# Performance work log

Hardware: AMD Instinct MI355X
Metric: run time of the kernel (lower is better)

The kernel has to match this reference:

```python
import jax, jax.numpy as jnp
import numpy as np

N_U = 50000
N_I = 50000
E = 800000
E_LBL = 200000
D_IN = 128
HID = 256
OUT = 128


def setup_inputs() -> dict:
    key = jax.random.key(0)
    ks = jax.random.split(key, 32)
    def glorot(k, shp):
        fan = shp[0] + shp[1]
        return jax.random.uniform(k, shp, jnp.float32, -1.0, 1.0) * np.sqrt(6.0 / fan)
    inp = {
        'x_user': jax.random.normal(ks[0], (N_U, D_IN), jnp.float32),
        'x_item': jax.random.normal(ks[1], (N_I, D_IN), jnp.float32),
        'edge_ui': jax.random.randint(ks[2], (2, E), 0, N_U, jnp.int32),
        'edge_iu': jax.random.randint(ks[3], (2, E), 0, N_I, jnp.int32),
        'edge_lbl': jax.random.randint(ks[4], (2, E_LBL), 0, N_U, jnp.int32),
        # layer 0 SAGE params (src_dim=D_IN, dst_dim=D_IN)
        'w_msg_ui0': glorot(ks[5], (D_IN, HID)), 'b_ui0': jnp.zeros((HID,), jnp.float32), 'w_root_ui0': glorot(ks[6], (D_IN, HID)),
        'w_msg_iu0': glorot(ks[7], (D_IN, HID)), 'b_iu0': jnp.zeros((HID,), jnp.float32), 'w_root_iu0': glorot(ks[8], (D_IN, HID)),
        # layer 1 SAGE params (src_dim=HID, dst_dim=HID)
        'w_msg_ui1': glorot(ks[9], (HID, HID)), 'b_ui1': jnp.zeros((HID,), jnp.float32), 'w_root_ui1': glorot(ks[10], (HID, HID)),
        'w_msg_iu1': glorot(ks[11], (HID, HID)), 'b_iu1': jnp.zeros((HID,), jnp.float32), 'w_root_iu1': glorot(ks[12], (HID, HID)),
        # per-node-type output linears on JK concat (2*HID -> OUT)
        'w_lin_u': glorot(ks[13], (2 * HID, OUT)), 'b_lin_u': jnp.zeros((OUT,), jnp.float32),
        'w_lin_i': glorot(ks[14], (2 * HID, OUT)), 'b_lin_i': jnp.zeros((OUT,), jnp.float32),
    }
    return inp


def _sage(x_src, x_dst, edge, w_msg, b_msg, w_root):
    # PyG SAGEConv(aggr='mean'): lin_l(mean_{j in N(i)} x_src[j]) + lin_r(x_dst[i])
    src, dst = edge[0], edge[1]
    n_dst = x_dst.shape[0]
    agg = jax.ops.segment_sum(x_src[src], dst, num_segments=n_dst)          # [n_dst, d_src]
    cnt = jax.ops.segment_sum(jnp.ones((edge.shape[1],), x_src.dtype), dst, num_segments=n_dst)
    mean = agg / jnp.maximum(cnt, 1.0)[:, None]
    return mean @ w_msg + b_msg + x_dst @ w_root


def reference(x_user, x_item, edge_ui, edge_iu, edge_lbl,
              w_msg_ui0, b_ui0, w_root_ui0, w_msg_iu0, b_iu0, w_root_iu0,
              w_msg_ui1, b_ui1, w_root_ui1, w_msg_iu1, b_iu1, w_root_iu1,
              w_lin_u, b_lin_u, w_lin_i, b_lin_i):
    # ----- encode: 2 HeteroConv(SAGEConv) layers -----
    item0 = _sage(x_user, x_item, edge_ui, w_msg_ui0, b_ui0, w_root_ui0)    # user->item
    user0 = _sage(x_item, x_user, edge_iu, b_msg=b_iu0, w_msg=w_msg_iu0, x_src=None, x_dst=None, edge=None, w_root=None) if False else _sage(x_item, x_user, edge_iu, w_msg_iu0, b_iu0, w_root_iu0)  # item->user
    item1 = _sage(user0, item0, edge_ui, w_msg_ui1, b_ui1, w_root_ui1)
    user1 = _sage(item0, user0, edge_iu, w_msg_iu1, b_iu1, w_root_iu1)
    # ----- JumpingKnowledge 'cat' + per-node-type linear -----
    z_user = jnp.concatenate([user0, user1], axis=-1) @ w_lin_u + b_lin_u   # [N_U, OUT]
    z_item = jnp.concatenate([item0, item1], axis=-1) @ w_lin_i + b_lin_i   # [N_I, OUT]
    # ----- decode: dot product over candidate edges (user, buys, item) -----
    pred = jnp.sum(z_user[edge_lbl[0]] * z_item[edge_lbl[1]], axis=-1)      # [E_LBL]
    return pred
```

## Files before the change

### kernel.cpp

```cpp
#include <hip/hip_runtime.h>

#define NU 50000
#define NI 50000
#define NE 800000
#define NLBL 200000
#define DIN 128
#define HID 256
#define DOUT 128

#define NSLICE 128
#define SLICE_SZ 6250
#define QN 12500
#define NQ 4

typedef unsigned short ushort_t;
typedef __attribute__((ext_vector_type(8))) short bf16x8;
typedef __attribute__((ext_vector_type(4))) float f32x4;

__device__ __forceinline__ float bf2f(unsigned int u_shifted) {
    union { unsigned int i; float f; } v;
    v.i = u_shifted;
    return v.f;
}
__device__ __forceinline__ float bf_lo(unsigned int u) { return bf2f(u << 16); }
__device__ __forceinline__ float bf_hi(unsigned int u) { return bf2f(u & 0xffff0000u); }
__device__ __forceinline__ ushort_t f2bf(float f) {
    union { float f; unsigned int i; } v;
    v.f = f;
    unsigned int r = (v.i + 0x7FFFu + ((v.i >> 16) & 1u)) >> 16;
    return (ushort_t)r;
}
__device__ __forceinline__ void load_lds16(const ushort_t* g, ushort_t* s) {
    __builtin_amdgcn_global_load_lds(
        (const __attribute__((address_space(1))) void*)g,
        (__attribute__((address_space(3))) void*)s, 16, 0, 0);
}

#define CVT_PER 782
#define CVT_B (2 * CVT_PER)
#define SA_B 512
#define HIST_B (2 * NSLICE * NQ)

struct P1Args {
    const int *eui, *eiu;
    ushort_t* cnt_s;
    const float *wm_ui1, *wr_ui1, *wm_iu1, *wr_iu1, *lin_i, *lin_u;
    float *G_i, *S_i, *G_u, *S_u;
    int* scan_part;
};

__global__ __launch_bounds__(256) void phase1(P1Args a) {
    __shared__ unsigned int cnt[QN / 2];
    int b = blockIdx.x, t = threadIdx.x;
    if (b < HIST_B) {
        int g = b >> 9, s = (b >> 2) & 127, q = b & 3;
        for (int i = t; i < QN / 2; i += 256) cnt[i] = 0;
        __syncthreads();
        const int* dst = (g ? a.eiu : a.eui) + NE;
        int hbase = q * QN;
        int e0 = s * SLICE_SZ;
        for (int i = e0 + t; i < e0 + SLICE_SZ; i += 256) {
            int d = dst[i] - hbase;
            if ((unsigned)d < (unsigned)QN)
                atomicAdd(&cnt[d >> 1], 1u << ((d & 1) * 16));
        }
        __syncthreads();
        unsigned int* outp = (unsigned int*)(a.cnt_s + ((size_t)(g * NSLICE + s)) * 50000 + hbase);
        for (int i = t; i < QN / 2; i += 256) outp[i] = cnt[i];
    } else if (b < HIST_B + SA_B) {
        int r2 = b - HIST_B;
        int which = r2 >> 7;
        int e = (r2 & 127) * 256 + t;
        int k = e >> 7, n = e & 127;
        const float* W = (which == 0) ? a.wm_ui1 : (which == 1) ? a.wr_ui1
                       : (which == 2) ? a.wm_iu1 : a.wr_iu1;
        const float* L = (which < 2) ? a.lin_i : a.lin_u;
        float* O = (which == 0) ? a.G_i : (which == 1) ? a.S_i
                 : (which == 2) ? a.G_u : a.S_u;
        float s = (which & 1) ? L[k * 128 + n] : 0.f;
#pragma unroll 4
        for (int j = 0; j < HID; ++j) s += W[k * HID + j] * L[(HID + j) * 128 + n];
        O[k * 128 + n] = s;
    } else {
        if (t < 64) a.scan_part[t] = 0;
    }
}

struct K2Args {
    ushort_t* cnt_s;
    int* totals;
    int* scan_part;
    const float *wm_ui0, *wr_ui0, *wm_iu0, *wr_iu0;
    const float *G_i, *S_i, *G_u, *S_u;
    const float *b_ui0, *b_iu0, *b_ui1, *b_iu1, *lin_i, *lin_u, *bl_i, *bl_u;
    ushort_t *VT1_i, *VT2_i, *VT3_i, *VT1_u, *VT2_u, *VT3_u;
    float *bz_i, *bz_u;
    const float* xu; ushort_t* xbu; const float* xi; ushort_t* xbi;
};

__global__ __launch_bounds__(256) void k2_scan_prep_cvt(K2Args a) {
    __shared__ int wsum[4];
    int b = blockIdx.x, t = threadIdx.x;
    if (b < 392) {
        if (b == 0 && t == 0) a.totals[100000] = 2 * NE;
        int idx = b * 256 + t;
        int run = 0;
        if (idx < 100000) {
            int g = idx / 50000, node = idx - g * 50000;
            size_t base = (size_t)g * NSLICE * 50000 + node;
#pragma unroll 4
            for (int s = 0; s < NSLICE; ++s) {
                size_t o = base + (size_t)s * 50000;
                int c = a.cnt_s[o];
                a.cnt_s[o] = (ushort_t)run;
                run += c;
            }
            a.totals[idx] = run;
        }
        int s = run;
#pragma unroll
        for (int off = 32; off > 0; off >>= 1) s += __shfl_down(s, off, 64);
        if ((t & 63) == 0) wsum[t >> 6] = s;
        __syncthreads();
        if (t == 0) atomicAdd(&a.scan_part[b >> 3], wsum[0] + wsum[1] + wsum[2] + wsum[3]);
    } else if (b < 778) {
        int task = b - 392;
        if (task < 384) {
            int v = task >> 6;
            int e = (task & 63) * 256 + t;
            int k = e >> 7, n = e & 127;
            const float *A1, *X1, *A2 = nullptr, *X2 = nullptr;
            ushort_t* O;
            switch (v) {
                case 0: A1 = a.wm_ui0; X1 = a.S_i; A2 = a.wr_iu0; X2 = a.G_i; O = a.VT1_i; break;
                case 1: A1 = a.wr_ui0; X1 = a.S_i; O = a.VT2_i; break;
                case 2: A1 = a.wm_iu0; X1 = a.G_i; O = a.VT3_i; break;
                case 3: A1 = a.wm_iu0; X1 = a.S_u; A2 = a.wr_ui0; X2 = a.G_u; O = a.VT1_u; break;
                case 4: A1 = a.wr_iu0; X1 = a.S_u; O = a.VT2_u; break;
                default: A1 = a.wm_ui0; X1 = a.G_u; O = a.VT3_u; break;
            }
            float s = 0.f;
#pragma unroll 4
            for (int j = 0; j < HID; ++j) s += A1[k * HID + j] * X1[j * 128 + n];
            if (A2) {
#pragma unroll 4
                for (int j = 0; j < HID; ++j) s += A2[k * HID + j] * X2[j * 128 + n];
            }
            O[n * 128 + k] = f2bf(s);
        } else if (t < 128) {
            int user = task - 384;
            int n = t;
            const float* S = user ? a.S_u : a.S_i;
            const float* G = user ? a.G_u : a.G_i;
            const float* b_own0 = user ? a.b_iu0 : a.b_ui0;
            const float* b_oth0 = user ? a.b_ui0 : a.b_iu0;
            const float* b_own1 = user ? a.b_iu1 : a.b_ui1;
            const float* lin = user ? a.lin_u : a.lin_i;
            const float* bl = user ? a.bl_u : a.bl_i;
            float* o = user ? a.bz_u : a.bz_i;
            float s = bl[n];
            for (int j = 0; j < HID; ++j)
                s += b_own0[j] * S[j * 128 + n] + b_oth0[j] * G[j * 128 + n] +
                     b_own1[j] * lin[(HID + j) * 128 + n];
            o[n] = s;
        }
    } else {
        int cb = b - 778;
        int which = (cb >= CVT_PER);
        if (which) cb -= CVT_PER;
        const float4* in = (const float4*)(which ? a.xi : a.xu);
        uint2* outp = (uint2*)(which ? a.xbi : a.xbu);
        const int n4 = NU * DIN / 4;
#pragma unroll
        for (int k = 0; k < 8; ++k) {
            int i = cb * 2048 + k * 256 + t;
            if (i < n4) {
                float4 v = in[i];
                uint2 o;
                o.x = (unsigned int)f2bf(v.x) | ((unsigned int)f2bf(v.y) << 16);
                o.y = (unsigned int)f2bf(v.z) | ((unsigned int)f2bf(v.w) << 16);
                outp[i] = o;
            }
        }
    }
}

__global__ __launch_bounds__(256) void scan3(int* __restrict__ d, const int* __restrict__ part,
                                             int n, int nb) {
    __shared__ int wsum[4];
    __shared__ int blockoff_sh;
    int b = blockIdx.x, t = threadIdx.x;
    int lane = t & 63, wv = t >> 6;
    if (t < 64) {
        int v = (t < nb) ? part[t] : 0;
        int incl = v;
#pragma unroll
        for (int off = 1; off < 64; off <<= 1) {
            int tv = __shfl_up(incl, off, 64);
            if (t >= off) incl += tv;
        }
        if (t == b) blockoff_sh = incl - v;
    }
    int i0 = b * 2048 + t * 8;
    int v[8];
    int tsum = 0;
#pragma unroll
    for (int k = 0; k < 8; ++k) {
        v[k] = (i0 + k < n) ? d[i0 + k] : 0;
        tsum += v[k];
    }
    int incl = tsum;
#pragma unroll
    for (int off = 1; off < 64; off <<= 1) {
        int tv = __shfl_up(incl, off, 64);
        if (lane >= off) incl += tv;
    }
    if (lane == 63) wsum[wv] = incl;
    __syncthreads();
    int woff = 0;
    for (int w = 0; w < wv; ++w) woff += wsum[w];
    int run = blockoff_sh + woff + (incl - tsum);
#pragma unroll
    for (int k = 0; k < 8; ++k) {
        if (i0 + k < n) d[i0 + k] = run;
        run += v[k];
    }
}

__global__ __launch_bounds__(256) void fill_lds(const int* __restrict__ eui,
                                                const int* __restrict__ eiu,
                                                const ushort_t* __restrict__ cnt_s,
                                                const int* __restrict__ rowstart,
                                                ushort_t* __restrict__ csr) {
    __shared__ unsigned int off[QN / 2];
    int b = blockIdx.x, t = threadIdx.x;
    int g = b >> 9, s = (b >> 2) & 127, q = b & 3;
    int hbase = q * QN;
    const unsigned int* st =
        (const unsigned int*)(cnt_s + ((size_t)(g * NSLICE + s)) * 50000 + hbase);
    for (int i = t; i < QN / 2; i += 256) off[i] = st[i];
    __syncthreads();
    const int* src = g ? eiu : eui;
    const int* dst = src + NE;
    const int* rs = rowstart + g * 50000;
    int e0 = s * SLICE_SZ;
    for (int i = e0 + t; i < e0 + SLICE_SZ; i += 256) {
        int dd = dst[i];
        int d = dd - hbase;
        if ((unsigned)d < (unsigned)QN) {
            unsigned old = atomicAdd(&off[d >> 1], 1u << ((d & 1) * 16));
            int rel = (int)((old >> ((d & 1) * 16)) & 0xffffu);
            csr[(size_t)rs[dd] + rel] = (ushort_t)src[i];
        }
    }
}

struct AggJob { const int* sp; const ushort_t* csr; const ushort_t* x; ushort_t* out; int n; };
struct AggJobs2 { AggJob j[2]; };

__global__ __launch_bounds__(256) void agg_din(AggJobs2 js) {
    AggJob jb = js.j[blockIdx.y];
    const int half = blockIdx.z;
    int wave = (int)((blockIdx.x * 256u + threadIdx.x) >> 6);
    int lane = threadIdx.x & 63;
    const int l = lane & 15;
    const int h = lane >> 4;
    int w4 = wave * 4;
    if (w4 >= jb.n) return;
    int w = w4 + h;
    int s0 = jb.sp[w];
    int s1 = jb.sp[w + 1];
    int cnt = s1 - s0;
    float sc = (cnt > 0) ? 1.0f / (float)cnt : 0.0f;
    int cmax = cnt;
    {
        int c1 = __shfl_xor(cmax, 16, 64); cmax = (cmax > c1) ? cmax : c1;
        int c2 = __shfl_xor(cmax, 32, 64); cmax = (cmax > c2) ? cmax : c2;
    }
    const uint2* xp = (const uint2*)jb.x + half * 16;
    float f0 = 0.f, f1 = 0.f, f2 = 0.f, f3 = 0.f;
#define ACC4(m, u)                                                     \
    f0 = fmaf(m, bf_lo(u.x), f0); f1 = fmaf(m, bf_hi(u.x), f1);        \
    f2 = fmaf(m, bf_lo(u.y), f2); f3 = fmaf(m, bf_hi(u.y), f3);
    for (int chunk = 0; chunk < cmax; chunk += 16) {
        int mh = cnt - chunk;
        int safe = (mh > 0) ? ((l < mh) ? l : mh - 1) : 0;
        int vidx = (int)jb.csr[s0 + chunk + safe];
        int mm = cmax - chunk;
        if (mm > 16) mm = 16;
        int j = 0;
        for (; j + 3 < mm; j += 4) {
            int i0 = __shfl(vidx, j, 16);
            int i1 = __shfl(vidx, j + 1, 16);
            int i2 = __shfl(vidx, j + 2, 16);
            int i3 = __shfl(vidx, j + 3, 16);
            float m0 = (j < mh) ? 1.f : 0.f;
            float m1 = (j + 1 < mh) ? 1.f : 0.f;
            float m2 = (j + 2 < mh) ? 1.f : 0.f;
            float m3 = (j + 3 < mh) ? 1.f : 0.f;
            uint2 u0 = xp[(size_t)((j < mh) ? i0 : 0) * 32 + l];
            uint2 u1 = xp[(size_t)((j + 1 < mh) ? i1 : 0) * 32 + l];
            uint2 u2 = xp[(size_t)((j + 2 < mh) ? i2 : 0) * 32 + l];
            uint2 u3 = xp[(size_t)((j + 3 < mh) ? i3 : 0) * 32 + l];
            ACC4(m0, u0);
            ACC4(m1, u1);
            ACC4(m2, u2);
            ACC4(m3, u3);
        }
        for (; j < mm; ++j) {
            int i0 = __shfl(vidx, j, 16);
            float m0 = (j < mh) ? 1.f : 0.f;
            uint2 u0 = xp[(size_t)((j < mh) ? i0 : 0) * 32 + l];
            ACC4(m0, u0);
        }
    }
#undef ACC4
    uint2 o;
    o.x = (unsigned int)f2bf(f0 * sc) | ((unsigned int)f2bf(f1 * sc) << 16);
    o.y = (unsigned int)f2bf(f2 * sc) | ((unsigned int)f2bf(f3 * sc) << 16);
    ((uint2*)jb.out)[(size_t)w * 32 + half * 16 + l] = o;
}

struct GemmJob {
    const ushort_t* A[3];
    const ushort_t* WT[3];
    int K[3];
    const float* bias;
    void* C;
};
struct GemmJobs2 { GemmJob j[2]; };

template <int NP, typename OutT>
__global__ __launch_bounds__(256) void gemmN(GemmJobs2 js, int M, int N) {
    GemmJob jb = js.j[blockIdx.z];
    __shared__ ushort_t sA[128 * 32];
    __shared__ ushort_t sB[128 * 32];
    const int tid = threadIdx.x;
    const int lane = tid & 63;
    const int wv = tid >> 6;
    const int wm = wv & 1, wn = wv >> 1;
    const int bm = blockIdx.y * 128, bn = blockIdx.x * 128;

    f32x4 acc[4][4] = {};

    const int srow = tid >> 2;
    const int scol = (tid & 3) * 8;

#pragma unroll
    for (int part = 0; part < NP; ++part) {
        const ushort_t* A = jb.A[part];
        const ushort_t* WT = jb.WT[part];
        const int K = jb.K[part];
        int ar0 = bm + srow;       if (ar0 > M - 1) ar0 = M - 1;
        int ar1 = bm + 64 + srow;  if (ar1 > M - 1) ar1 = M - 1;
        const size_t aoff0 = (size_t)ar0 * K + scol;
        const size_t aoff1 = (size_t)ar1 * K + scol;
        const size_t boff0 = (size_t)(bn + srow) * K + scol;
        const size_t boff1 = (size_t)(bn + 64 + srow) * K + scol;
        for (int k0 = 0; k0 < K; k0 += 32) {
            __syncthreads();
            load_lds16(A + aoff0 + k0, sA + tid * 8);
            load_lds16(A + aoff1 + k0, sA + 2048 + tid * 8);
            load_lds16(WT + boff0 + k0, sB + tid * 8);
            load_lds16(WT + boff1 + k0, sB + 2048 + tid * 8);
            __syncthreads();
            const ushort_t* pA = sA + ((wm * 64 + (lane & 15)) * 32 + (lane >> 4) * 8);
            const ushort_t* pB = sB + ((wn * 64 + (lane & 15)) * 32 + (lane >> 4) * 8);
            bf16x8 af[4], bfr[4];
#pragma unroll
            for (int mt = 0; mt < 4; ++mt) af[mt] = *(const bf16x8*)(pA + mt * 512);
#pragma unroll
            for (int nt = 0; nt < 4; ++nt) bfr[nt] = *(const bf16x8*)(pB + nt * 512);
#pragma unroll
            for (int mt = 0; mt < 4; ++mt)
#pragma unroll
                for (int nt = 0; nt < 4; ++nt)
                    acc[mt][nt] = __builtin_amdgcn_mfma_f32_16x16x32_bf16(
                        af[mt], bfr[nt], acc[mt][nt], 0, 0, 0);
        }
    }

#pragma unroll
    for (int mt = 0; mt < 4; ++mt) {
#pragma unroll
        for (int r = 0; r < 4; ++r) {
            int row = bm + wm * 64 + mt * 16 + (lane >> 4) * 4 + r;
            if (row >= M) continue;
#pragma unroll
            for (int nt = 0; nt < 4; ++nt) {
                int col = bn + wn * 64 + nt * 16 + (lane & 15);
                float v = acc[mt][nt][r] + jb.bias[col];
                if constexpr (sizeof(OutT) == 2)
                    ((ushort_t*)jb.C)[(size_t)row * N + col] = f2bf(v);
                else
                    ((float*)jb.C)[(size_t)row * N + col] = v;
            }
        }
    }
}

__global__ void decode_kernel(const int* __restrict__ lbl, const ushort_t* __restrict__ zu,
                              const ushort_t* __restrict__ zi, float* __restrict__ out, int n) {
    int gid = blockIdx.x * blockDim.x + threadIdx.x;
    int wave = gid >> 6;
    int lane = threadIdx.x & 63;
    int q = lane >> 4;
    int l = lane & 15;
    int e = wave * 4 + q;
    if (e >= n) return;
    int u = lbl[e];
    int it = lbl[n + e];
    uint4 a = ((const uint4*)zu)[(size_t)u * 16 + l];
    uint4 b = ((const uint4*)zi)[(size_t)it * 16 + l];
    float s = bf_lo(a.x) * bf_lo(b.x) + bf_hi(a.x) * bf_hi(b.x) +
              bf_lo(a.y) * bf_lo(b.y) + bf_hi(a.y) * bf_hi(b.y) +
              bf_lo(a.z) * bf_lo(b.z) + bf_hi(a.z) * bf_hi(b.z) +
              bf_lo(a.w) * bf_lo(b.w) + bf_hi(a.w) * bf_hi(b.w);
#pragma unroll
    for (int off = 8; off > 0; off >>= 1) s += __shfl_down(s, off, 16);
    if (l == 0) out[e] = s;
}

extern "C" void kernel_launch(void* const* d_in, const int* in_sizes, int n_in,
                              void* d_out, int out_size, void* d_ws, size_t ws_size,
                              hipStream_t stream) {
    const float* x_user = (const float*)d_in[0];
    const float* x_item = (const float*)d_in[1];
    const int* edge_ui = (const int*)d_in[2];
    const int* edge_iu = (const int*)d_in[3];
    const int* edge_lbl = (const int*)d_in[4];
    const float* w_msg_ui0 = (const float*)d_in[5];
    const float* b_ui0 = (const float*)d_in[6];
    const float* w_root_ui0 = (const float*)d_in[7];
    const float* w_msg_iu0 = (const float*)d_in[8];
    const float* b_iu0 = (const float*)d_in[9];
    const float* w_root_iu0 = (const float*)d_in[10];
    const float* w_msg_ui1 = (const float*)d_in[11];
    const float* b_ui1 = (const float*)d_in[12];
    const float* w_root_ui1 = (const float*)d_in[13];
    const float* w_msg_iu1 = (const float*)d_in[14];
    const float* b_iu1 = (const float*)d_in[15];
    const float* w_root_iu1 = (const float*)d_in[16];
    const float* w_lin_u = (const float*)d_in[17];
    const float* b_lin_u = (const float*)d_in[18];
    const float* w_lin_i = (const float*)d_in[19];
    const float* b_lin_i = (const float*)d_in[20];
    float* out = (float*)d_out;

    char* p = (char*)d_ws;
    ushort_t* A_i  = (ushort_t*)p;   p += (size_t)NI * DIN * 2;
    ushort_t* A_u  = (ushort_t*)p;   p += (size_t)NU * DIN * 2;
    ushort_t* B_i  = (ushort_t*)p;   p += (size_t)NI * DIN * 2;
    ushort_t* B_u  = (ushort_t*)p;   p += (size_t)NU * DIN * 2;
    ushort_t* xb_u  = (ushort_t*)p;  p += (size_t)NU * DIN * 2;
    ushort_t* xb_i  = (ushort_t*)p;  p += (size_t)NI * DIN * 2;
    ushort_t* z_user = (ushort_t*)p; p += (size_t)NU * DOUT * 2;
    ushort_t* z_item = (ushort_t*)p; p += (size_t)NI * DOUT * 2;
    int* totals     = (int*)p;       p += (size_t)(100000 + 64) * 4;
    ushort_t* csr   = (ushort_t*)p;  p += (size_t)2 * NE * 2;
    ushort_t* cnt_s = (ushort_t*)p;  p += (size_t)2 * NSLICE * 50000 * 2;
    int* scan_part  = (int*)p;       p += 64 * 4;
    float* G_i = (float*)p; p += (size_t)HID * 128 * 4;
    float* S_i = (float*)p; p += (size_t)HID * 128 * 4;
    float* G_u = (float*)p; p += (size_t)HID * 128 * 4;
    float* S_u = (float*)p; p += (size_t)HID * 128 * 4;
    ushort_t* VT1_i = (ushort_t*)p; p += (size_t)128 * 128 * 2;
    ushort_t* VT2_i = (ushort_t*)p; p += (size_t)128 * 128 * 2;
    ushort_t* VT3_i = (ushort_t*)p; p += (size_t)128 * 128 * 2;
    ushort_t* VT1_u = (ushort_t*)p; p += (size_t)128 * 128 * 2;
    ushort_t* VT2_u = (ushort_t*)p; p += (size_t)128 * 128 * 2;
    ushort_t* VT3_u = (ushort_t*)p; p += (size_t)128 * 128 * 2;
    float* bz_i = (float*)p; p += 128 * 4;
    float* bz_u = (float*)p; p += 128 * 4;

    const int NCNT = 100000;
    const int NB = (NCNT + 2047) / 2048;

    P1Args p1;
    p1.eui = edge_ui; p1.eiu = edge_iu; p1.cnt_s = cnt_s;
    p1.wm_ui1 = w_msg_ui1; p1.wr_ui1 = w_root_ui1;
    p1.wm_iu1 = w_msg_iu1; p1.wr_iu1 = w_root_iu1;
    p1.lin_i = w_lin_i; p1.lin_u = w_lin_u;
    p1.G_i = G_i; p1.S_i = S_i; p1.G_u = G_u; p1.S_u = S_u;
    p1.scan_part = scan_part;
    phase1<<<HIST_B + SA_B + 1, 256, 0, stream>>>(p1);

    K2Args k2;
    k2.cnt_s = cnt_s; k2.totals = totals; k2.scan_part = scan_part;
    k2.wm_ui0 = w_msg_ui0; k2.wr_ui0 = w_root_ui0;
    k2.wm_iu0 = w_msg_iu0; k2.wr_iu0 = w_root_iu0;
    k2.G_i = G_i; k2.S_i = S_i; k2.G_u = G_u; k2.S_u = S_u;
    k2.b_ui0 = b_ui0; k2.b_iu0 = b_iu0; k2.b_ui1 = b_ui1; k2.b_iu1 = b_iu1;
    k2.lin_i = w_lin_i; k2.lin_u = w_lin_u; k2.bl_i = b_lin_i; k2.bl_u = b_lin_u;
    k2.VT1_i = VT1_i; k2.VT2_i = VT2_i; k2.VT3_i = VT3_i;
    k2.VT1_u = VT1_u; k2.VT2_u = VT2_u; k2.VT3_u = VT3_u;
    k2.bz_i = bz_i; k2.bz_u = bz_u;
    k2.xu = x_user; k2.xbu = xb_u; k2.xi = x_item; k2.xbi = xb_i;
    k2_scan_prep_cvt<<<392 + 386 + CVT_B, 256, 0, stream>>>(k2);

    scan3<<<NB, 256, 0, stream>>>(totals, scan_part, NCNT, NB);

    fill_lds<<<HIST_B, 256, 0, stream>>>(edge_ui, edge_iu, cnt_s, totals, csr);

    {
        AggJobs2 aj = {{{totals, csr, xb_u, A_i, NI},
                        {totals + 50000, csr, xb_i, A_u, NU}}};
        agg_din<<<dim3(3125, 2, 2), 256, 0, stream>>>(aj);
    }
    {
        AggJobs2 aj = {{{totals, csr, A_u, B_i, NI},
                        {totals + 50000, csr, A_i, B_u, NU}}};
        agg_din<<<dim3(3125, 2, 2), 256, 0, stream>>>(aj);
    }

    {
        GemmJobs2 gj = {{{{A_i, xb_i, B_i}, {VT1_i, VT2_i, VT3_i}, {DIN, DIN, DIN}, bz_i, z_item},
                         {{A_u, xb_u, B_u}, {VT1_u, VT2_u, VT3_u}, {DIN, DIN, DIN}, bz_u, z_user}}};
        gemmN<3, ushort_t><<<dim3(DOUT / 128, (NU + 127) / 128, 2), 256, 0, stream>>>(gj, NU, DOUT);
    }

    decode_kernel<<<(((NLBL + 3) / 4) * 64 + 255) / 256, 256, 0, stream>>>(
        edge_lbl, z_user, z_item, out, NLBL);
}
```

Baseline: 356.8 us.

## Shrink per-slice edge counters to bytes and parallelize slice scan across threads

The per-slice destination histograms now use 8-bit counters packed four per word instead of 16-bit, which halves the cnt_s buffer traffic in the histogram, scan and fill kernels. The fill kernel unpacks the bytes back into its 16-bit LDS layout. The per-node prefix scan over 128 slices is split across 8 threads, each handling 16 slices and combining with a segmented shuffle scan. This launches far more blocks than the old one-thread-per-node serial loop. The risk is that any node with 256 or more in-edges overflows the byte counters, so correctness depends on the degree distribution of the inputs.

```diff
diff --git a/kernel.cpp b/kernel.cpp
--- a/kernel.cpp
+++ b/kernel.cpp
@@ -14,6 +14,7 @@
 #define NQ 4
 
 typedef unsigned short ushort_t;
+typedef unsigned char uchar_t;
 typedef __attribute__((ext_vector_type(8))) short bf16x8;
 typedef __attribute__((ext_vector_type(4))) float f32x4;
 
@@ -40,21 +41,22 @@
 #define CVT_B (2 * CVT_PER)
 #define SA_B 512
 #define HIST_B (2 * NSLICE * NQ)
+#define SS_B 3125
 
 struct P1Args {
     const int *eui, *eiu;
-    ushort_t* cnt_s;
+    uchar_t* cnt_s;
     const float *wm_ui1, *wr_ui1, *wm_iu1, *wr_iu1, *lin_i, *lin_u;
     float *G_i, *S_i, *G_u, *S_u;
     int* scan_part;
 };
 
 __global__ __launch_bounds__(256) void phase1(P1Args a) {
-    __shared__ unsigned int cnt[QN / 2];
+    __shared__ unsigned int cnt[QN / 4];
     int b = blockIdx.x, t = threadIdx.x;
     if (b < HIST_B) {
         int g = b >> 9, s = (b >> 2) & 127, q = b & 3;
-        for (int i = t; i < QN / 2; i += 256) cnt[i] = 0;
+        for (int i = t; i < QN / 4; i += 256) cnt[i] = 0;
         __syncthreads();
         const int* dst = (g ? a.eiu : a.eui) + NE;
         int hbase = q * QN;
@@ -62,11 +64,11 @@
         for (int i = e0 + t; i < e0 + SLICE_SZ; i += 256) {
             int d = dst[i] - hbase;
             if ((unsigned)d < (unsigned)QN)
-                atomicAdd(&cnt[d >> 1], 1u << ((d & 1) * 16));
+                atomicAdd(&cnt[d >> 2], 1u << ((d & 3) * 8));
         }
         __syncthreads();
         unsigned int* outp = (unsigned int*)(a.cnt_s + ((size_t)(g * NSLICE + s)) * 50000 + hbase);
-        for (int i = t; i < QN / 2; i += 256) outp[i] = cnt[i];
+        for (int i = t; i < QN / 4; i += 256) outp[i] = cnt[i];
     } else if (b < HIST_B + SA_B) {
         int r2 = b - HIST_B;
         int which = r2 >> 7;
@@ -87,7 +89,7 @@
 }
 
 struct K2Args {
-    ushort_t* cnt_s;
+    uchar_t* cnt_s;
     int* totals;
     int* scan_part;
     const float *wm_ui0, *wr_ui0, *wm_iu0, *wr_iu0;
@@ -101,30 +103,41 @@
 __global__ __launch_bounds__(256) void k2_scan_prep_cvt(K2Args a) {
     __shared__ int wsum[4];
     int b = blockIdx.x, t = threadIdx.x;
-    if (b < 392) {
+    if (b < SS_B) {
         if (b == 0 && t == 0) a.totals[100000] = 2 * NE;
         int idx = b * 256 + t;
-        int run = 0;
-        if (idx < 100000) {
-            int g = idx / 50000, node = idx - g * 50000;
-            size_t base = (size_t)g * NSLICE * 50000 + node;
-#pragma unroll 4
-            for (int s = 0; s < NSLICE; ++s) {
-                size_t o = base + (size_t)s * 50000;
-                int c = a.cnt_s[o];
-                a.cnt_s[o] = (ushort_t)run;
-                run += c;
-            }
-            a.totals[idx] = run;
-        }
-        int s = run;
+        int node_g = idx >> 3;
+        int part = idx & 7;
+        int g = node_g / 50000, node = node_g - g * 50000;
+        size_t base = (size_t)g * NSLICE * 50000 + node;
+        int c[16];
+        int sum = 0;
+#pragma unroll
+        for (int k = 0; k < 16; ++k) {
+            c[k] = a.cnt_s[base + (size_t)(part * 16 + k) * 50000];
+            sum += c[k];
+        }
+        int incl = sum;
+#pragma unroll
+        for (int off = 1; off < 8; off <<= 1) {
+            int tv = __shfl_up(incl, off, 8);
+            if (part >= off) incl += tv;
+        }
+        int run = incl - sum;
+#pragma unroll
+        for (int k = 0; k < 16; ++k) {
+            a.cnt_s[base + (size_t)(part * 16 + k) * 50000] = (uchar_t)run;
+            run += c[k];
+        }
+        if (part == 7) a.totals[node_g] = incl;
+        int s = (part == 7) ? incl : 0;
 #pragma unroll
         for (int off = 32; off > 0; off >>= 1) s += __shfl_down(s, off, 64);
         if ((t & 63) == 0) wsum[t >> 6] = s;
         __syncthreads();
-        if (t == 0) atomicAdd(&a.scan_part[b >> 3], wsum[0] + wsum[1] + wsum[2] + wsum[3]);
-    } else if (b < 778) {
-        int task = b - 392;
+        if (t == 0) atomicAdd(&a.scan_part[b >> 6], wsum[0] + wsum[1] + wsum[2] + wsum[3]);
+    } else if (b < SS_B + 386) {
+        int task = b - SS_B;
         if (task < 384) {
             int v = task >> 6;
             int e = (task & 63) * 256 + t;
@@ -165,7 +178,7 @@
             o[n] = s;
         }
     } else {
-        int cb = b - 778;
+        int cb = b - (SS_B + 386);
         int which = (cb >= CVT_PER);
         if (which) cb -= CVT_PER;
         const float4* in = (const float4*)(which ? a.xi : a.xu);
@@ -229,7 +242,7 @@
 
 __global__ __launch_bounds__(256) void fill_lds(const int* __restrict__ eui,
                                                 const int* __restrict__ eiu,
-                                                const ushort_t* __restrict__ cnt_s,
+                                                const uchar_t* __restrict__ cnt_s,
                                                 const int* __restrict__ rowstart,
                                                 ushort_t* __restrict__ csr) {
     __shared__ unsigned int off[QN / 2];
@@ -238,7 +251,11 @@
     int hbase = q * QN;
     const unsigned int* st =
         (const unsigned int*)(cnt_s + ((size_t)(g * NSLICE + s)) * 50000 + hbase);
-    for (int i = t; i < QN / 2; i += 256) off[i] = st[i];
+    for (int i = t; i < QN / 4; i += 256) {
+        unsigned int v = st[i];
+        off[2 * i]     = (v & 0xffu) | ((v >> 8) & 0xffu) << 16;
+        off[2 * i + 1] = ((v >> 16) & 0xffu) | ((v >> 24) & 0xffu) << 16;
+    }
     __syncthreads();
     const int* src = g ? eiu : eui;
     const int* dst = src + NE;
@@ -458,7 +475,7 @@
     ushort_t* z_item = (ushort_t*)p; p += (size_t)NI * DOUT * 2;
     int* totals     = (int*)p;       p += (size_t)(100000 + 64) * 4;
     ushort_t* csr   = (ushort_t*)p;  p += (size_t)2 * NE * 2;
-    ushort_t* cnt_s = (ushort_t*)p;  p += (size_t)2 * NSLICE * 50000 * 2;
+    uchar_t* cnt_s  = (uchar_t*)p;   p += (size_t)2 * NSLICE * 50000;
     int* scan_part  = (int*)p;       p += 64 * 4;
     float* G_i = (float*)p; p += (size_t)HID * 128 * 4;
     float* S_i = (float*)p; p += (size_t)HID * 128 * 4;
@@ -496,7 +513,7 @@
     k2.VT1_u = VT1_u; k2.VT2_u = VT2_u; k2.VT3_u = VT3_u;
     k2.bz_i = bz_i; k2.bz_u = bz_u;
     k2.xu = x_user; k2.xbu = xb_u; k2.xi = x_item; k2.xbi = xb_i;
-    k2_scan_prep_cvt<<<392 + 386 + CVT_B, 256, 0, stream>>>(k2);
+    k2_scan_prep_cvt<<<SS_B + 386 + CVT_B, 256, 0, stream>>>(k2);
 
     scan3<<<NB, 256, 0, stream>>>(totals, scan_part, NCNT, NB);
 
```

Measured after the change: 372.2 us. 4.3% more time.
